# Kernel tuning notes

Hardware: AMD Instinct MI355X
Metric: run time of the kernel (lower is better)

The kernel has to match this reference:

```python
import jax, jax.numpy as jnp
import numpy as np

B, N, M, D, H = 2, 2048, 2048, 1024, 16
HD = D // H          # head_dim = 64
F = int(D * 4.0)     # mlp hidden = 4096
EPS = 1e-5


def layernorm(x, w, b):
    mu = jnp.mean(x, axis=-1, keepdims=True)
    var = jnp.mean(jnp.square(x - mu), axis=-1, keepdims=True)
    return (x - mu) * jax.lax.rsqrt(var + EPS) * w + b


def setup_inputs() -> dict:
    key = jax.random.key(0)
    ks = jax.random.split(key, 8)
    w = lambda k, shape: jax.random.normal(k, shape, dtype=jnp.float32) * 0.02
    return {
        "query": jax.random.normal(ks[0], (B, N, D), dtype=jnp.float32),
        "context": jax.random.normal(ks[1], (B, M, D), dtype=jnp.float32),
        "qpos": jax.random.randint(ks[2], (B, N), 0, N, dtype=jnp.int32),
        "cpos": jax.random.randint(ks[3], (B, M), 0, M, dtype=jnp.int32),
        "Wq_w": w(ks[4], (D, D)), "Wq_b": jnp.zeros((D,), jnp.float32),
        "Wk_w": w(ks[5], (D, D)), "Wk_b": jnp.zeros((D,), jnp.float32),
        "Wv_w": w(ks[6], (D, D)), "Wv_b": jnp.zeros((D,), jnp.float32),
        "qn_w": jnp.ones((HD,), jnp.float32), "qn_b": jnp.zeros((HD,), jnp.float32),
        "kn_w": jnp.ones((HD,), jnp.float32), "kn_b": jnp.zeros((HD,), jnp.float32),
        "ffn_w": jnp.ones((D,), jnp.float32), "ffn_b": jnp.zeros((D,), jnp.float32),
        "fc1_w": w(ks[7], (D, F)), "fc1_b": jnp.zeros((F,), jnp.float32),
        "fc2_w": w(jax.random.fold_in(key, 99), (F, D)), "fc2_b": jnp.zeros((D,), jnp.float32),
    }


def reference(query, context, qpos, cpos,
              Wq_w, Wq_b, Wk_w, Wk_b, Wv_w, Wv_b,
              qn_w, qn_b, kn_w, kn_b,
              ffn_w, ffn_b, fc1_w, fc1_b, fc2_w, fc2_b):
    # rope=None -> qpos/cpos unused (kept for signature fidelity)
    res = query
    # QKV projections, split heads -> (B,H,T,HD)
    Q = (query @ Wq_w + Wq_b).reshape(B, N, H, HD).transpose(0, 2, 1, 3)
    K = (context @ Wk_w + Wk_b).reshape(B, M, H, HD).transpose(0, 2, 1, 3)
    V = (context @ Wv_w + Wv_b).reshape(B, M, H, HD).transpose(0, 2, 1, 3)
    # per-head LayerNorm on q and k
    Q = layernorm(Q, qn_w, qn_b)
    K = layernorm(K, kn_w, kn_b)
    # attention
    scores = jnp.einsum('bhnd,bhmd->bhnm', Q, K) / jnp.sqrt(jnp.float32(HD))
    attn = jax.nn.softmax(scores, axis=-1)
    out = jnp.einsum('bhnm,bhmd->bhnd', attn, V)
    out = out.transpose(0, 2, 1, 3).reshape(B, N, D)
    out = res + out
    # MLP block with pre-norm
    res2 = out
    h = layernorm(out, ffn_w, ffn_b)
    h = jax.nn.gelu(h @ fc1_w + fc1_b, approximate=False)
    h = h @ fc2_w + fc2_b
    return res2 + h
```

## Files before the change

kernel.cpp:

```cpp
#include <hip/hip_runtime.h>
#include <hip/hip_bf16.h>
#include <math.h>

constexpr int Bb  = 2;
constexpr int Nn  = 2048;
constexpr int Mm  = 2048;
constexpr int Dd  = 1024;
constexpr int Hh  = 16;
constexpr int HD  = 64;
constexpr int Ff  = 4096;
constexpr float EPS = 1e-5f;
constexpr float QSCALE = 0.125f * 1.4426950408889634f;
constexpr float SMAX = 12.0f;

typedef __attribute__((ext_vector_type(8))) short bf16x8;
typedef __attribute__((ext_vector_type(4))) short bf16x4;
typedef __attribute__((ext_vector_type(4))) float f32x4;

__device__ inline unsigned short f2bf(float f) {
    __hip_bfloat16 h = __float2bfloat16(f);
    return *reinterpret_cast<unsigned short*>(&h);
}
__device__ inline unsigned short f2bf_rh(float f) {
    union { float f; unsigned u; } c{f};
    return (unsigned short)((c.u + 0x8000u) >> 16);
}
__device__ inline float bf2f(unsigned short u) {
    union { unsigned u; float f; } c{(unsigned)u << 16};
    return c.f;
}

__device__ inline float gelu_fast(float x) {
    float t = x * x;
    float f = fmaf(-0.10295004f, t, -2.30211782f);
    float e = __builtin_amdgcn_exp2f(x * f);
    return x * __builtin_amdgcn_rcpf(1.0f + e);
}

__device__ inline void async_load16(const void* g, void* l) {
    __builtin_amdgcn_global_load_lds(
        (const __attribute__((address_space(1))) void*)g,
        (__attribute__((address_space(3))) void*)l, 16, 0, 0);
}

__device__ inline bf16x8 ld_b64x2(const unsigned short* p) {
    bf16x4 lo = *(const bf16x4*)p;
    bf16x4 hi = *(const bf16x4*)(p + 4);
    bf16x8 r;
#pragma unroll
    for (int i = 0; i < 4; i++) { r[i] = lo[i]; r[i + 4] = hi[i]; }
    return r;
}

__global__ __launch_bounds__(256) void prep_kernel(
    const float* __restrict__ query, const float* __restrict__ context,
    unsigned short* __restrict__ qa, unsigned short* __restrict__ ca,
    const float* __restrict__ W0, const float* __restrict__ W1,
    const float* __restrict__ W2, const float* __restrict__ W3,
    const float* __restrict__ W4,
    unsigned short* __restrict__ T0, unsigned short* __restrict__ T1,
    unsigned short* __restrict__ T2, unsigned short* __restrict__ T3,
    unsigned short* __restrict__ T4)
{
    __shared__ float tile[32][33];
    int bid = blockIdx.x;
    if (bid < 8192) {
        int i = bid * 256 + threadIdx.x;
        const float* x; unsigned short* y; int k;
        if (i < 1048576) { x = query; y = qa; k = i; }
        else { x = context; y = ca; k = i - 1048576; }
        float4 v = reinterpret_cast<const float4*>(x)[k];
        ushort4 o;
        o.x = f2bf(v.x); o.y = f2bf(v.y); o.z = f2bf(v.z); o.w = f2bf(v.w);
        reinterpret_cast<ushort4*>(y)[k] = o;
        return;
    }
    bid -= 8192;
    const float* W; unsigned short* T; int K, Cn, tid;
    if (bid < 3072) {
        int j = bid >> 10; tid = bid & 1023;
        W = (j == 0) ? W0 : (j == 1) ? W1 : W2;
        T = (j == 0) ? T0 : (j == 1) ? T1 : T2;
        K = Dd; Cn = Dd;
    } else if (bid < 7168) {
        tid = bid - 3072; W = W3; T = T3; K = Dd; Cn = Ff;
    } else {
        tid = bid - 7168; W = W4; T = T4; K = Ff; Cn = Dd;
    }
    int xt = Cn >> 5;
    int bx = tid % xt, by = tid / xt;
    int tx = threadIdx.x & 31, ty = threadIdx.x >> 5;
    int c = bx * 32 + tx;
    int kbase = by * 32;
#pragma unroll
    for (int i = ty; i < 32; i += 8)
        tile[i][tx] = W[(size_t)(kbase + i) * Cn + c];
    __syncthreads();
    int k = kbase + tx;
#pragma unroll
    for (int i = ty; i < 32; i += 8)
        T[(size_t)(bx * 32 + i) * K + k] = f2bf(tile[tx][i]);
}

__global__ __launch_bounds__(256) void qkv_fused_kernel(
    const unsigned short* __restrict__ qa, const unsigned short* __restrict__ ca,
    const unsigned short* __restrict__ Wqt, const unsigned short* __restrict__ Wkt,
    const unsigned short* __restrict__ Wvt,
    const float* __restrict__ bq, const float* __restrict__ bk,
    const float* __restrict__ bv,
    const float* __restrict__ qn_w, const float* __restrict__ qn_b,
    const float* __restrict__ kn_w, const float* __restrict__ kn_b,
    unsigned short* __restrict__ Qbh, unsigned short* __restrict__ Kbh,
    unsigned short* __restrict__ Vt_g)
{
    __shared__ __align__(16) unsigned short As[128 * 32];
    __shared__ __align__(16) unsigned short Bs[128 * 32];

    const int bz = blockIdx.z;
    const unsigned short* A  = (bz == 0) ? qa : ca;
    const unsigned short* Bt = (bz == 0) ? Wqt : (bz == 1) ? Wkt : Wvt;
    const float* bias        = (bz == 0) ? bq  : (bz == 1) ? bk  : bv;
    const int K = Dd;

    const int t    = threadIdx.x;
    const int wave = t >> 6;
    const int lane = t & 63;
    const int r0 = blockIdx.y * 128;
    const int c0 = blockIdx.x * 128;
    const int wm = (wave >> 1) * 64;
    const int wn = (wave & 1) * 64;

    f32x4 acc[4][4];
#pragma unroll
    for (int i = 0; i < 4; i++)
#pragma unroll
        for (int j = 0; j < 4; j++) acc[i][j] = (f32x4)0.0f;

    const int row1 = t >> 2, kc = (t & 3) * 8;
    const size_t arow1 = (size_t)(r0 + row1) * K;
    const size_t arow2 = (size_t)(r0 + row1 + 64) * K;
    const size_t brow1 = (size_t)(c0 + row1) * K;
    const size_t brow2 = (size_t)(c0 + row1 + 64) * K;
    char* AsB1 = (char*)As + wave * 1024;
    char* AsB2 = (char*)As + 4096 + wave * 1024;
    char* BsB1 = (char*)Bs + wave * 1024;
    char* BsB2 = (char*)Bs + 4096 + wave * 1024;

    const int m  = lane & 15;
    const int kq = (lane >> 4) * 8;

    for (int k0 = 0; k0 < K; k0 += 32) {
        async_load16(A + arow1 + k0 + kc, AsB1);
        async_load16(A + arow2 + k0 + kc, AsB2);
        async_load16(Bt + brow1 + k0 + kc, BsB1);
        async_load16(Bt + brow2 + k0 + kc, BsB2);
        __syncthreads();

        bf16x8 af[4], bfr[4];
#pragma unroll
        for (int mi = 0; mi < 4; mi++)
            af[mi] = *(const bf16x8*)&As[(wm + mi * 16 + m) * 32 + kq];
#pragma unroll
        for (int nj = 0; nj < 4; nj++)
            bfr[nj] = *(const bf16x8*)&Bs[(wn + nj * 16 + m) * 32 + kq];
#pragma unroll
        for (int mi = 0; mi < 4; mi++)
#pragma unroll
            for (int nj = 0; nj < 4; nj++)
                acc[mi][nj] = __builtin_amdgcn_mfma_f32_16x16x32_bf16(
                    af[mi], bfr[nj], acc[mi][nj], 0, 0, 0);
        __syncthreads();
    }

    const int rowb = r0 + wm + (lane >> 4) * 4;
    const int colb = c0 + wn + m;
#pragma unroll
    for (int nj = 0; nj < 4; nj++) {
        float bvv = bias[colb + nj * 16];
#pragma unroll
        for (int mi = 0; mi < 4; mi++)
#pragma unroll
            for (int r = 0; r < 4; r++) acc[mi][nj][r] += bvv;
    }

    if (bz < 2) {
        unsigned short* O = (bz == 0) ? Qbh : Kbh;
        const float* lw = (bz == 0) ? qn_w : kn_w;
        const float* lb = (bz == 0) ? qn_b : kn_b;
        const float scale = (bz == 0) ? QSCALE : 1.0f;
        const int hcol = c0 + wn;
        float w4[4], b4[4];
#pragma unroll
        for (int nj = 0; nj < 4; nj++) {
            int d = nj * 16 + m;
            w4[nj] = lw[d]; b4[nj] = lb[d];
        }
#pragma unroll
        for (int mi = 0; mi < 4; mi++) {
#pragma unroll
            for (int r = 0; r < 4; r++) {
                float s = (acc[mi][0][r] + acc[mi][1][r]) +
                          (acc[mi][2][r] + acc[mi][3][r]);
                s += __shfl_xor(s, 1); s += __shfl_xor(s, 2);
                s += __shfl_xor(s, 4); s += __shfl_xor(s, 8);
                float mu = s * (1.0f / 64.0f);
                float v2 = 0.f;
#pragma unroll
                for (int nj = 0; nj < 4; nj++) {
                    float dd = acc[mi][nj][r] - mu; v2 += dd * dd;
                }
                v2 += __shfl_xor(v2, 1); v2 += __shfl_xor(v2, 2);
                v2 += __shfl_xor(v2, 4); v2 += __shfl_xor(v2, 8);
                float rstd = rsqrtf(v2 * (1.0f / 64.0f) + EPS);
                size_t base = (size_t)(rowb + mi * 16 + r) * Dd + hcol;
#pragma unroll
                for (int nj = 0; nj < 4; nj++) {
                    int d = nj * 16 + m;
                    O[base + d] = f2bf(
                        ((acc[mi][nj][r] - mu) * rstd * w4[nj] + b4[nj]) * scale);
                }
            }
        }
    } else {
#pragma unroll
        for (int mi = 0; mi < 4; mi++) {
            int row0 = rowb + mi * 16;
            int bidx = row0 >> 11;
            int mtok = row0 & (Mm - 1);
#pragma unroll
            for (int nj = 0; nj < 4; nj++) {
                int col = colb + nj * 16;
                int h = col >> 6, d = col & 63;
                ushort4 o;
                o.x = f2bf(acc[mi][nj][0]);
                o.y = f2bf(acc[mi][nj][1]);
                o.z = f2bf(acc[mi][nj][2]);
                o.w = f2bf(acc[mi][nj][3]);
                *(ushort4*)(Vt_g + (((size_t)(bidx * Hh + h) * HD + d) << 11) + mtok) = o;
            }
        }
    }
}

template <int EPI, int OUTBF>
__global__ __launch_bounds__(256) void gemm_mfma_bt(
    const unsigned short* __restrict__ A,
    const unsigned short* __restrict__ Bt,
    const float* __restrict__ bias, const float* __restrict__ resid,
    void* __restrict__ Cout, int R, int K, int Cn)
{
    __shared__ __align__(16) unsigned short As[128 * 32];
    __shared__ __align__(16) unsigned short Bs[128 * 32];

    const int t    = threadIdx.x;
    const int wave = t >> 6;
    const int lane = t & 63;
    const int r0 = blockIdx.y * 128;
    const int c0 = blockIdx.x * 128;
    const int wm = (wave >> 1) * 64;
    const int wn = (wave & 1) * 64;

    f32x4 acc[4][4];
#pragma unroll
    for (int i = 0; i < 4; i++)
#pragma unroll
        for (int j = 0; j < 4; j++) acc[i][j] = (f32x4)0.0f;

    const int row1 = t >> 2, kc = (t & 3) * 8;
    const size_t arow1 = (size_t)(r0 + row1) * K;
    const size_t arow2 = (size_t)(r0 + row1 + 64) * K;
    const size_t brow1 = (size_t)(c0 + row1) * K;
    const size_t brow2 = (size_t)(c0 + row1 + 64) * K;
    char* AsB1 = (char*)As + wave * 1024;
    char* AsB2 = (char*)As + 4096 + wave * 1024;
    char* BsB1 = (char*)Bs + wave * 1024;
    char* BsB2 = (char*)Bs + 4096 + wave * 1024;

    const int m  = lane & 15;
    const int kq = (lane >> 4) * 8;

    for (int k0 = 0; k0 < K; k0 += 32) {
        async_load16(A + arow1 + k0 + kc, AsB1);
        async_load16(A + arow2 + k0 + kc, AsB2);
        async_load16(Bt + brow1 + k0 + kc, BsB1);
        async_load16(Bt + brow2 + k0 + kc, BsB2);
        __syncthreads();

        bf16x8 af[4], bfr[4];
#pragma unroll
        for (int mi = 0; mi < 4; mi++)
            af[mi] = *(const bf16x8*)&As[(wm + mi * 16 + m) * 32 + kq];
#pragma unroll
        for (int nj = 0; nj < 4; nj++)
            bfr[nj] = *(const bf16x8*)&Bs[(wn + nj * 16 + m) * 32 + kq];
#pragma unroll
        for (int mi = 0; mi < 4; mi++)
#pragma unroll
            for (int nj = 0; nj < 4; nj++)
                acc[mi][nj] = __builtin_amdgcn_mfma_f32_16x16x32_bf16(
                    af[mi], bfr[nj], acc[mi][nj], 0, 0, 0);
        __syncthreads();
    }

    const int rowb = r0 + wm + (lane >> 4) * 4;
    const int colb = c0 + wn + m;
#pragma unroll
    for (int mi = 0; mi < 4; mi++) {
#pragma unroll
        for (int nj = 0; nj < 4; nj++) {
            int col = colb + nj * 16;
            float bv = bias[col];
#pragma unroll
            for (int r = 0; r < 4; r++) {
                int row = rowb + mi * 16 + r;
                float v = acc[mi][nj][r] + bv;
                if (EPI == 1) v = gelu_fast(v);
                if (resid) v += resid[(size_t)row * Cn + col];
                if (OUTBF)
                    ((unsigned short*)Cout)[(size_t)row * Cn + col] = f2bf(v);
                else
                    ((float*)Cout)[(size_t)row * Cn + col] = v;
            }
        }
    }
}

__global__ __launch_bounds__(256) void gemm_fc2_split(
    const unsigned short* __restrict__ A,
    const unsigned short* __restrict__ Bt,
    unsigned short* __restrict__ Part)
{
    constexpr int Kfull = Ff;
    constexpr int Ksub  = Ff / 4;
    constexpr int Cn    = Dd;
    const int split = blockIdx.z;
    const int koff  = split * Ksub;

    __shared__ __align__(16) unsigned short As[128 * 32];
    __shared__ __align__(16) unsigned short Bs[128 * 32];

    const int t    = threadIdx.x;
    const int wave = t >> 6;
    const int lane = t & 63;
    const int r0 = blockIdx.y * 128;
    const int c0 = blockIdx.x * 128;
    const int wm = (wave >> 1) * 64;
    const int wn = (wave & 1) * 64;

    f32x4 acc[4][4];
#pragma unroll
    for (int i = 0; i < 4; i++)
#pragma unroll
        for (int j = 0; j < 4; j++) acc[i][j] = (f32x4)0.0f;

    const int row1 = t >> 2, kc = (t & 3) * 8;
    const size_t arow1 = (size_t)(r0 + row1) * Kfull + koff;
    const size_t arow2 = (size_t)(r0 + row1 + 64) * Kfull + koff;
    const size_t brow1 = (size_t)(c0 + row1) * Kfull + koff;
    const size_t brow2 = (size_t)(c0 + row1 + 64) * Kfull + koff;
    char* AsB1 = (char*)As + wave * 1024;
    char* AsB2 = (char*)As + 4096 + wave * 1024;
    char* BsB1 = (char*)Bs + wave * 1024;
    char* BsB2 = (char*)Bs + 4096 + wave * 1024;

    const int m  = lane & 15;
    const int kq = (lane >> 4) * 8;

    for (int k0 = 0; k0 < Ksub; k0 += 32) {
        async_load16(A + arow1 + k0 + kc, AsB1);
        async_load16(A + arow2 + k0 + kc, AsB2);
        async_load16(Bt + brow1 + k0 + kc, BsB1);
        async_load16(Bt + brow2 + k0 + kc, BsB2);
        __syncthreads();

        bf16x8 af[4], bfr[4];
#pragma unroll
        for (int mi = 0; mi < 4; mi++)
            af[mi] = *(const bf16x8*)&As[(wm + mi * 16 + m) * 32 + kq];
#pragma unroll
        for (int nj = 0; nj < 4; nj++)
            bfr[nj] = *(const bf16x8*)&Bs[(wn + nj * 16 + m) * 32 + kq];
#pragma unroll
        for (int mi = 0; mi < 4; mi++)
#pragma unroll
            for (int nj = 0; nj < 4; nj++)
                acc[mi][nj] = __builtin_amdgcn_mfma_f32_16x16x32_bf16(
                    af[mi], bfr[nj], acc[mi][nj], 0, 0, 0);
        __syncthreads();
    }

    unsigned short* P = Part + (size_t)split * ((size_t)Bb * Nn * Dd);
    const int rowb = r0 + wm + (lane >> 4) * 4;
    const int colb = c0 + wn + m;
#pragma unroll
    for (int mi = 0; mi < 4; mi++)
#pragma unroll
        for (int nj = 0; nj < 4; nj++) {
            int col = colb + nj * 16;
#pragma unroll
            for (int r = 0; r < 4; r++)
                P[(size_t)(rowb + mi * 16 + r) * Cn + col] = f2bf(acc[mi][nj][r]);
        }
}

__global__ __launch_bounds__(256) void fc2_reduce_kernel(
    const unsigned short* __restrict__ Part, const float* __restrict__ bias,
    const float* __restrict__ attn, float* __restrict__ out)
{
    constexpr size_t NEl = (size_t)Bb * Nn * Dd;
    size_t i4 = (size_t)blockIdx.x * 256 + threadIdx.x;
    size_t i = i4 * 4;
    float4 s = *reinterpret_cast<const float4*>(attn + i);
    float4 bv = *reinterpret_cast<const float4*>(bias + (i & (Dd - 1)));
    s.x += bv.x; s.y += bv.y; s.z += bv.z; s.w += bv.w;
#pragma unroll
    for (int sp = 0; sp < 4; sp++) {
        ushort4 u = *reinterpret_cast<const ushort4*>(Part + sp * NEl + i);
        s.x += bf2f(u.x); s.y += bf2f(u.y); s.z += bf2f(u.z); s.w += bf2f(u.w);
    }
    *reinterpret_cast<float4*>(out + i) = s;
}

__global__ __launch_bounds__(256) void ln_row_bf16_kernel(
    const float* __restrict__ X, const float* __restrict__ w,
    const float* __restrict__ b, unsigned short* __restrict__ Y)
{
    int row = blockIdx.x;
    const float* x = X + (size_t)row * Dd;
    int t = threadIdx.x;
    float v[4];
    float s = 0.f;
#pragma unroll
    for (int i = 0; i < 4; i++) { v[i] = x[t + i * 256]; s += v[i]; }
#pragma unroll
    for (int off = 32; off; off >>= 1) s += __shfl_xor(s, off);
    __shared__ float red[4];
    __shared__ float stats[2];
    if ((t & 63) == 0) red[t >> 6] = s;
    __syncthreads();
    if (t == 0) stats[0] = (red[0] + red[1] + red[2] + red[3]) * (1.0f / Dd);
    __syncthreads();
    float mu = stats[0];
    float s2 = 0.f;
#pragma unroll
    for (int i = 0; i < 4; i++) { float d = v[i] - mu; s2 += d * d; }
#pragma unroll
    for (int off = 32; off; off >>= 1) s2 += __shfl_xor(s2, off);
    __syncthreads();
    if ((t & 63) == 0) red[t >> 6] = s2;
    __syncthreads();
    if (t == 0) stats[1] = (red[0] + red[1] + red[2] + red[3]) * (1.0f / Dd);
    __syncthreads();
    float rstd = rsqrtf(stats[1] + EPS);
    unsigned short* y = Y + (size_t)row * Dd;
#pragma unroll
    for (int i = 0; i < 4; i++) {
        int c = t + i * 256;
        y[c] = f2bf((v[i] - mu) * rstd * w[c] + b[c]);
    }
}

__global__ __launch_bounds__(512) void attention_mfma_kernel(
    const unsigned short* __restrict__ Qb,
    const unsigned short* __restrict__ Kb,
    const unsigned short* __restrict__ Vt_g,
    const float* __restrict__ query,
    float* __restrict__ Out)
{
    const int bid = blockIdx.x;
    const int g  = bid & 31;
    const int qt = bid >> 5;
    const int b  = g >> 4;
    const int h  = g & 15;
    const int q0 = qt * 128;

    __shared__ __align__(16) unsigned short Ks[2][2 * 64 * 32];
    __shared__ __align__(16) unsigned short Vts[2][2 * 64 * 32];
    __shared__ __align__(16) unsigned short Ps[8 * 16 * 68];

    const int t    = threadIdx.x;
    const int wave = t >> 6;
    const int lane = t & 63;
    const int m16  = lane & 15;
    const int kg   = lane >> 4;
    const int swc  = (kg ^ ((m16 >> 1) & 3)) << 3;

    bf16x8 qf[2];
    {
        const unsigned short* qp =
            Qb + ((size_t)(b * Nn + q0 + wave * 16 + m16) * Dd + h * HD + kg * 8);
        qf[0] = *(const bf16x8*)qp;
        qf[1] = *(const bf16x8*)(qp + 32);
    }

    f32x4 oacc[4];
    float lrow[4];
#pragma unroll
    for (int i = 0; i < 4; i++) { oacc[i] = (f32x4)0.f; lrow[i] = 0.f; }

    const size_t kbase  = (size_t)(b * Mm) * Dd + h * HD;
    const size_t vtbase = ((size_t)(b * Hh + h) * HD) * Mm;
    unsigned short* psw = Ps + wave * (16 * 68);

    const int u    = t & 255;
    const int pan  = t >> 8;
    const int srow = u >> 2;
    const int schk = ((u & 3) ^ ((srow >> 1) & 3)) * 8;
    char* kdstA = (char*)&Ks[0][0]  + pan * 4096 + (wave & 3) * 1024;
    char* kdstB = (char*)&Ks[1][0]  + pan * 4096 + (wave & 3) * 1024;
    char* vdstA = (char*)&Vts[0][0] + pan * 4096 + (wave & 3) * 1024;
    char* vdstB = (char*)&Vts[1][0] + pan * 4096 + (wave & 3) * 1024;
    const unsigned short* kp0 = Kb + kbase + (size_t)srow * Dd + schk + pan * 32;
    const unsigned short* vp0 = Vt_g + vtbase + (size_t)srow * Mm + schk + pan * 32;

    async_load16(kp0, kdstA);
    async_load16(vp0, vdstA);

    for (int m0 = 0; m0 < Mm; m0 += 64) {
        __syncthreads();
        const int cur = (m0 >> 6) & 1;
        if (m0 + 64 < Mm) {
            async_load16(kp0 + (size_t)(m0 + 64) * Dd, cur ? kdstA : kdstB);
            async_load16(vp0 + (m0 + 64),              cur ? vdstA : vdstB);
        }
        const unsigned short* Kc = &Ks[cur][0];
        const unsigned short* Vc = &Vts[cur][0];

        f32x4 s[4];
#pragma unroll
        for (int j = 0; j < 4; j++) {
            bf16x8 b0 = *(const bf16x8*)&Kc[(j * 16 + m16) * 32 + swc];
            bf16x8 b1 = *(const bf16x8*)&Kc[2048 + (j * 16 + m16) * 32 + swc];
            f32x4 a = (f32x4)(-SMAX);
            a = __builtin_amdgcn_mfma_f32_16x16x32_bf16(qf[0], b0, a, 0, 0, 0);
            a = __builtin_amdgcn_mfma_f32_16x16x32_bf16(qf[1], b1, a, 0, 0, 0);
            s[j] = a;
        }

#pragma unroll
        for (int r = 0; r < 4; r++) {
            float p0 = __builtin_amdgcn_exp2f(s[0][r]);
            float p1 = __builtin_amdgcn_exp2f(s[1][r]);
            float p2 = __builtin_amdgcn_exp2f(s[2][r]);
            float p3 = __builtin_amdgcn_exp2f(s[3][r]);
            lrow[r] += (p0 + p1) + (p2 + p3);
            int qrow = kg * 4 + r;
            psw[qrow * 68 +  0 + m16] = f2bf_rh(p0);
            psw[qrow * 68 + 16 + m16] = f2bf_rh(p1);
            psw[qrow * 68 + 32 + m16] = f2bf_rh(p2);
            psw[qrow * 68 + 48 + m16] = f2bf_rh(p3);
        }

        bf16x8 pf0 = ld_b64x2(psw + m16 * 68 + kg * 8);
        bf16x8 pf1 = ld_b64x2(psw + m16 * 68 + 32 + kg * 8);
#pragma unroll
        for (int dj = 0; dj < 4; dj++) {
            bf16x8 v0 = *(const bf16x8*)&Vc[(dj * 16 + m16) * 32 + swc];
            bf16x8 v1 = *(const bf16x8*)&Vc[2048 + (dj * 16 + m16) * 32 + swc];
            oacc[dj] = __builtin_amdgcn_mfma_f32_16x16x32_bf16(pf0, v0, oacc[dj], 0, 0, 0);
            oacc[dj] = __builtin_amdgcn_mfma_f32_16x16x32_bf16(pf1, v1, oacc[dj], 0, 0, 0);
        }
    }

#pragma unroll
    for (int r = 0; r < 4; r++) {
        float l = lrow[r];
        l += __shfl_xor(l, 1);
        l += __shfl_xor(l, 2);
        l += __shfl_xor(l, 4);
        l += __shfl_xor(l, 8);
        float inv = 1.0f / l;
        const size_t rowbase =
            (size_t)(b * Nn + q0 + wave * 16 + kg * 4 + r) * Dd + h * HD;
#pragma unroll
        for (int dj = 0; dj < 4; dj++) {
            size_t idx = rowbase + dj * 16 + m16;
            Out[idx] = query[idx] + oacc[dj][r] * inv;
        }
    }
}

extern "C" void kernel_launch(void* const* d_in, const int* in_sizes, int n_in,
                              void* d_out, int out_size, void* d_ws, size_t ws_size,
                              hipStream_t stream)
{
    const float* query   = (const float*)d_in[0];
    const float* context = (const float*)d_in[1];
    const float* Wq_w = (const float*)d_in[4];
    const float* Wq_b = (const float*)d_in[5];
    const float* Wk_w = (const float*)d_in[6];
    const float* Wk_b = (const float*)d_in[7];
    const float* Wv_w = (const float*)d_in[8];
    const float* Wv_b = (const float*)d_in[9];
    const float* qn_w = (const float*)d_in[10];
    const float* qn_b = (const float*)d_in[11];
    const float* kn_w = (const float*)d_in[12];
    const float* kn_b = (const float*)d_in[13];
    const float* ffn_w = (const float*)d_in[14];
    const float* ffn_b = (const float*)d_in[15];
    const float* fc1_w = (const float*)d_in[16];
    const float* fc1_b = (const float*)d_in[17];
    const float* fc2_w = (const float*)d_in[18];
    const float* fc2_b = (const float*)d_in[19];

    constexpr size_t BND = (size_t)Bb * Nn * Dd;
    constexpr size_t BMD = (size_t)Bb * Mm * Dd;
    constexpr size_t DD  = (size_t)Dd * Dd;
    constexpr size_t DF  = (size_t)Dd * Ff;

    const size_t need = BND * 4 + (2 * BND + 3 * BMD) * 2 + (3 * DD + 2 * DF) * 2
                      + 4 * BND * 2;
    if (ws_size < need) return;

    char* p = (char*)d_ws;
    float* attn = (float*)p;                   p += BND * 4;
    unsigned short* Qbh  = (unsigned short*)p; p += BND * 2;
    unsigned short* Kbh  = (unsigned short*)p; p += BMD * 2;
    unsigned short* Vt_g = (unsigned short*)p; p += BMD * 2;
    unsigned short* qa   = (unsigned short*)p; p += BND * 2;
    unsigned short* ca   = (unsigned short*)p; p += BMD * 2;
    unsigned short* Wqt  = (unsigned short*)p; p += DD * 2;
    unsigned short* Wkt  = (unsigned short*)p; p += DD * 2;
    unsigned short* Wvt  = (unsigned short*)p; p += DD * 2;
    unsigned short* fc1t = (unsigned short*)p; p += DF * 2;
    unsigned short* fc2t = (unsigned short*)p; p += DF * 2;
    unsigned short* part = (unsigned short*)p; p += 4 * BND * 2;
    unsigned short* normed = Qbh;
    unsigned short* mid    = Kbh;
    float* out = (float*)d_out;

    const int R = Bb * Nn;
    dim3 blk(256);

    prep_kernel<<<19456, blk, 0, stream>>>(
        query, context, qa, ca,
        Wq_w, Wk_w, Wv_w, fc1_w, fc2_w, Wqt, Wkt, Wvt, fc1t, fc2t);

    qkv_fused_kernel<<<dim3(Dd / 128, R / 128, 3), blk, 0, stream>>>(
        qa, ca, Wqt, Wkt, Wvt, Wq_b, Wk_b, Wv_b,
        qn_w, qn_b, kn_w, kn_b, Qbh, Kbh, Vt_g);

    attention_mfma_kernel<<<Bb * Hh * (Nn / 128), 512, 0, stream>>>(
        Qbh, Kbh, Vt_g, query, attn);

    ln_row_bf16_kernel<<<Bb * Nn, blk, 0, stream>>>(attn, ffn_w, ffn_b, normed);

    gemm_mfma_bt<1, 1><<<dim3(Ff / 128, R / 128), blk, 0, stream>>>(
        normed, fc1t, fc1_b, nullptr, mid, R, Dd, Ff);
    gemm_fc2_split<<<dim3(Dd / 128, R / 128, 4), blk, 0, stream>>>(
        mid, fc2t, part);
    fc2_reduce_kernel<<<BND / 4 / 256, blk, 0, stream>>>(
        part, fc2_b, attn, out);
}
```

Before: 377.0 us.

## Double-buffer LDS tiles and XOR-swizzle layout in all MFMA GEMM kernels

The QKV, generic and split-K fc2 GEMM kernels now keep two LDS buffers per operand. Each iteration prefetches the next K-slice into the other buffer before running the MFMAs on the current one, which also drops one __syncthreads per iteration. The global load offsets and the LDS fragment reads use a matching XOR swizzle of the 16-byte chunks, meant to cut LDS bank conflicts. The cost is twice the LDS per block (32 KB), which may reduce occupancy.

Result: faster. 367.3 us (-2.6%).

```diff
diff --git a/kernel.cpp b/kernel.cpp
--- a/kernel.cpp
+++ b/kernel.cpp
@@ -113,8 +113,8 @@
     unsigned short* __restrict__ Qbh, unsigned short* __restrict__ Kbh,
     unsigned short* __restrict__ Vt_g)
 {
-    __shared__ __align__(16) unsigned short As[128 * 32];
-    __shared__ __align__(16) unsigned short Bs[128 * 32];
+    __shared__ __align__(16) unsigned short As[2][128 * 32];
+    __shared__ __align__(16) unsigned short Bs[2][128 * 32];
 
     const int bz = blockIdx.z;
     const unsigned short* A  = (bz == 0) ? qa : ca;
@@ -136,40 +136,55 @@
 #pragma unroll
         for (int j = 0; j < 4; j++) acc[i][j] = (f32x4)0.0f;
 
-    const int row1 = t >> 2, kc = (t & 3) * 8;
-    const size_t arow1 = (size_t)(r0 + row1) * K;
-    const size_t arow2 = (size_t)(r0 + row1 + 64) * K;
-    const size_t brow1 = (size_t)(c0 + row1) * K;
-    const size_t brow2 = (size_t)(c0 + row1 + 64) * K;
-    char* AsB1 = (char*)As + wave * 1024;
-    char* AsB2 = (char*)As + 4096 + wave * 1024;
-    char* BsB1 = (char*)Bs + wave * 1024;
-    char* BsB2 = (char*)Bs + 4096 + wave * 1024;
-
-    const int m  = lane & 15;
-    const int kq = (lane >> 4) * 8;
+    const int row1 = t >> 2;
+    const int kcs  = ((t & 3) ^ ((t >> 3) & 3)) * 8;
+    const size_t arow1 = (size_t)(r0 + row1) * K + kcs;
+    const size_t arow2 = (size_t)(r0 + row1 + 64) * K + kcs;
+    const size_t brow1 = (size_t)(c0 + row1) * K + kcs;
+    const size_t brow2 = (size_t)(c0 + row1 + 64) * K + kcs;
+    char* A1_0 = (char*)&As[0][0] + wave * 1024;
+    char* A2_0 = (char*)&As[0][0] + 4096 + wave * 1024;
+    char* B1_0 = (char*)&Bs[0][0] + wave * 1024;
+    char* B2_0 = (char*)&Bs[0][0] + 4096 + wave * 1024;
+    char* A1_1 = (char*)&As[1][0] + wave * 1024;
+    char* A2_1 = (char*)&As[1][0] + 4096 + wave * 1024;
+    char* B1_1 = (char*)&Bs[1][0] + wave * 1024;
+    char* B2_1 = (char*)&Bs[1][0] + 4096 + wave * 1024;
+
+    const int m   = lane & 15;
+    const int swc = ((lane >> 4) ^ ((m >> 1) & 3)) << 3;
+
+    async_load16(A + arow1, A1_0);
+    async_load16(A + arow2, A2_0);
+    async_load16(Bt + brow1, B1_0);
+    async_load16(Bt + brow2, B2_0);
 
     for (int k0 = 0; k0 < K; k0 += 32) {
-        async_load16(A + arow1 + k0 + kc, AsB1);
-        async_load16(A + arow2 + k0 + kc, AsB2);
-        async_load16(Bt + brow1 + k0 + kc, BsB1);
-        async_load16(Bt + brow2 + k0 + kc, BsB2);
         __syncthreads();
+        const int cur = (k0 >> 5) & 1;
+        if (k0 + 32 < K) {
+            const int nk = k0 + 32;
+            async_load16(A + arow1 + nk, cur ? A1_0 : A1_1);
+            async_load16(A + arow2 + nk, cur ? A2_0 : A2_1);
+            async_load16(Bt + brow1 + nk, cur ? B1_0 : B1_1);
+            async_load16(Bt + brow2 + nk, cur ? B2_0 : B2_1);
+        }
+        const unsigned short* Ac = &As[cur][0];
+        const unsigned short* Bc = &Bs[cur][0];
 
         bf16x8 af[4], bfr[4];
 #pragma unroll
         for (int mi = 0; mi < 4; mi++)
-            af[mi] = *(const bf16x8*)&As[(wm + mi * 16 + m) * 32 + kq];
+            af[mi] = *(const bf16x8*)&Ac[(wm + mi * 16 + m) * 32 + swc];
 #pragma unroll
         for (int nj = 0; nj < 4; nj++)
-            bfr[nj] = *(const bf16x8*)&Bs[(wn + nj * 16 + m) * 32 + kq];
+            bfr[nj] = *(const bf16x8*)&Bc[(wn + nj * 16 + m) * 32 + swc];
 #pragma unroll
         for (int mi = 0; mi < 4; mi++)
 #pragma unroll
             for (int nj = 0; nj < 4; nj++)
                 acc[mi][nj] = __builtin_amdgcn_mfma_f32_16x16x32_bf16(
                     af[mi], bfr[nj], acc[mi][nj], 0, 0, 0);
-        __syncthreads();
     }
 
     const int rowb = r0 + wm + (lane >> 4) * 4;
@@ -249,8 +264,8 @@
     const float* __restrict__ bias, const float* __restrict__ resid,
     void* __restrict__ Cout, int R, int K, int Cn)
 {
-    __shared__ __align__(16) unsigned short As[128 * 32];
-    __shared__ __align__(16) unsigned short Bs[128 * 32];
+    __shared__ __align__(16) unsigned short As[2][128 * 32];
+    __shared__ __align__(16) unsigned short Bs[2][128 * 32];
 
     const int t    = threadIdx.x;
     const int wave = t >> 6;
@@ -266,40 +281,55 @@
 #pragma unroll
         for (int j = 0; j < 4; j++) acc[i][j] = (f32x4)0.0f;
 
-    const int row1 = t >> 2, kc = (t & 3) * 8;
-    const size_t arow1 = (size_t)(r0 + row1) * K;
-    const size_t arow2 = (size_t)(r0 + row1 + 64) * K;
-    const size_t brow1 = (size_t)(c0 + row1) * K;
-    const size_t brow2 = (size_t)(c0 + row1 + 64) * K;
-    char* AsB1 = (char*)As + wave * 1024;
-    char* AsB2 = (char*)As + 4096 + wave * 1024;
-    char* BsB1 = (char*)Bs + wave * 1024;
-    char* BsB2 = (char*)Bs + 4096 + wave * 1024;
-
-    const int m  = lane & 15;
-    const int kq = (lane >> 4) * 8;
+    const int row1 = t >> 2;
+    const int kcs  = ((t & 3) ^ ((t >> 3) & 3)) * 8;
+    const size_t arow1 = (size_t)(r0 + row1) * K + kcs;
+    const size_t arow2 = (size_t)(r0 + row1 + 64) * K + kcs;
+    const size_t brow1 = (size_t)(c0 + row1) * K + kcs;
+    const size_t brow2 = (size_t)(c0 + row1 + 64) * K + kcs;
+    char* A1_0 = (char*)&As[0][0] + wave * 1024;
+    char* A2_0 = (char*)&As[0][0] + 4096 + wave * 1024;
+    char* B1_0 = (char*)&Bs[0][0] + wave * 1024;
+    char* B2_0 = (char*)&Bs[0][0] + 4096 + wave * 1024;
+    char* A1_1 = (char*)&As[1][0] + wave * 1024;
+    char* A2_1 = (char*)&As[1][0] + 4096 + wave * 1024;
+    char* B1_1 = (char*)&Bs[1][0] + wave * 1024;
+    char* B2_1 = (char*)&Bs[1][0] + 4096 + wave * 1024;
+
+    const int m   = lane & 15;
+    const int swc = ((lane >> 4) ^ ((m >> 1) & 3)) << 3;
+
+    async_load16(A + arow1, A1_0);
+    async_load16(A + arow2, A2_0);
+    async_load16(Bt + brow1, B1_0);
+    async_load16(Bt + brow2, B2_0);
 
     for (int k0 = 0; k0 < K; k0 += 32) {
-        async_load16(A + arow1 + k0 + kc, AsB1);
-        async_load16(A + arow2 + k0 + kc, AsB2);
-        async_load16(Bt + brow1 + k0 + kc, BsB1);
-        async_load16(Bt + brow2 + k0 + kc, BsB2);
         __syncthreads();
+        const int cur = (k0 >> 5) & 1;
+        if (k0 + 32 < K) {
+            const int nk = k0 + 32;
+            async_load16(A + arow1 + nk, cur ? A1_0 : A1_1);
+            async_load16(A + arow2 + nk, cur ? A2_0 : A2_1);
+            async_load16(Bt + brow1 + nk, cur ? B1_0 : B1_1);
+            async_load16(Bt + brow2 + nk, cur ? B2_0 : B2_1);
+        }
+        const unsigned short* Ac = &As[cur][0];
+        const unsigned short* Bc = &Bs[cur][0];
 
         bf16x8 af[4], bfr[4];
 #pragma unroll
         for (int mi = 0; mi < 4; mi++)
-            af[mi] = *(const bf16x8*)&As[(wm + mi * 16 + m) * 32 + kq];
+            af[mi] = *(const bf16x8*)&Ac[(wm + mi * 16 + m) * 32 + swc];
 #pragma unroll
         for (int nj = 0; nj < 4; nj++)
-            bfr[nj] = *(const bf16x8*)&Bs[(wn + nj * 16 + m) * 32 + kq];
+            bfr[nj] = *(const bf16x8*)&Bc[(wn + nj * 16 + m) * 32 + swc];
 #pragma unroll
         for (int mi = 0; mi < 4; mi++)
 #pragma unroll
             for (int nj = 0; nj < 4; nj++)
                 acc[mi][nj] = __builtin_amdgcn_mfma_f32_16x16x32_bf16(
                     af[mi], bfr[nj], acc[mi][nj], 0, 0, 0);
-        __syncthreads();
     }
 
     const int rowb = r0 + wm + (lane >> 4) * 4;
@@ -336,8 +366,8 @@
     const int split = blockIdx.z;
     const int koff  = split * Ksub;
 
-    __shared__ __align__(16) unsigned short As[128 * 32];
-    __shared__ __align__(16) unsigned short Bs[128 * 32];
+    __shared__ __align__(16) unsigned short As[2][128 * 32];
+    __shared__ __align__(16) unsigned short Bs[2][128 * 32];
 
     const int t    = threadIdx.x;
     const int wave = t >> 6;
@@ -353,40 +383,55 @@
 #pragma unroll
         for (int j = 0; j < 4; j++) acc[i][j] = (f32x4)0.0f;
 
-    const int row1 = t >> 2, kc = (t & 3) * 8;
-    const size_t arow1 = (size_t)(r0 + row1) * Kfull + koff;
-    const size_t arow2 = (size_t)(r0 + row1 + 64) * Kfull + koff;
-    const size_t brow1 = (size_t)(c0 + row1) * Kfull + koff;
-    const size_t brow2 = (size_t)(c0 + row1 + 64) * Kfull + koff;
-    char* AsB1 = (char*)As + wave * 1024;
-    char* AsB2 = (char*)As + 4096 + wave * 1024;
-    char* BsB1 = (char*)Bs + wave * 1024;
-    char* BsB2 = (char*)Bs + 4096 + wave * 1024;
-
-    const int m  = lane & 15;
-    const int kq = (lane >> 4) * 8;
+    const int row1 = t >> 2;
+    const int kcs  = ((t & 3) ^ ((t >> 3) & 3)) * 8;
+    const size_t arow1 = (size_t)(r0 + row1) * Kfull + koff + kcs;
+    const size_t arow2 = (size_t)(r0 + row1 + 64) * Kfull + koff + kcs;
+    const size_t brow1 = (size_t)(c0 + row1) * Kfull + koff + kcs;
+    const size_t brow2 = (size_t)(c0 + row1 + 64) * Kfull + koff + kcs;
+    char* A1_0 = (char*)&As[0][0] + wave * 1024;
+    char* A2_0 = (char*)&As[0][0] + 4096 + wave * 1024;
+    char* B1_0 = (char*)&Bs[0][0] + wave * 1024;
+    char* B2_0 = (char*)&Bs[0][0] + 4096 + wave * 1024;
+    char* A1_1 = (char*)&As[1][0] + wave * 1024;
+    char* A2_1 = (char*)&As[1][0] + 4096 + wave * 1024;
+    char* B1_1 = (char*)&Bs[1][0] + wave * 1024;
+    char* B2_1 = (char*)&Bs[1][0] + 4096 + wave * 1024;
+
+    const int m   = lane & 15;
+    const int swc = ((lane >> 4) ^ ((m >> 1) & 3)) << 3;
+
+    async_load16(A + arow1, A1_0);
+    async_load16(A + arow2, A2_0);
+    async_load16(Bt + brow1, B1_0);
+    async_load16(Bt + brow2, B2_0);
 
     for (int k0 = 0; k0 < Ksub; k0 += 32) {
-        async_load16(A + arow1 + k0 + kc, AsB1);
-        async_load16(A + arow2 + k0 + kc, AsB2);
-        async_load16(Bt + brow1 + k0 + kc, BsB1);
-        async_load16(Bt + brow2 + k0 + kc, BsB2);
         __syncthreads();
+        const int cur = (k0 >> 5) & 1;
+        if (k0 + 32 < Ksub) {
+            const int nk = k0 + 32;
+            async_load16(A + arow1 + nk, cur ? A1_0 : A1_1);
+            async_load16(A + arow2 + nk, cur ? A2_0 : A2_1);
+            async_load16(Bt + brow1 + nk, cur ? B1_0 : B1_1);
+            async_load16(Bt + brow2 + nk, cur ? B2_0 : B2_1);
+        }
+        const unsigned short* Ac = &As[cur][0];
+        const unsigned short* Bc = &Bs[cur][0];
 
         bf16x8 af[4], bfr[4];
 #pragma unroll
         for (int mi = 0; mi < 4; mi++)
-            af[mi] = *(const bf16x8*)&As[(wm + mi * 16 + m) * 32 + kq];
+            af[mi] = *(const bf16x8*)&Ac[(wm + mi * 16 + m) * 32 + swc];
 #pragma unroll
         for (int nj = 0; nj < 4; nj++)
-            bfr[nj] = *(const bf16x8*)&Bs[(wn + nj * 16 + m) * 32 + kq];
+            bfr[nj] = *(const bf16x8*)&Bc[(wn + nj * 16 + m) * 32 + swc];
 #pragma unroll
         for (int mi = 0; mi < 4; mi++)
 #pragma unroll
             for (int nj = 0; nj < 4; nj++)
                 acc[mi][nj] = __builtin_amdgcn_mfma_f32_16x16x32_bf16(
                     af[mi], bfr[nj], acc[mi][nj], 0, 0, 0);
-        __syncthreads();
     }
 
     unsigned short* P = Part + (size_t)split * ((size_t)Bb * Nn * Dd);
```
